# Kernel tuning notes

Measured on AMD Instinct MI355X. Metric: run time of the kernel, lower is better.

Reference implementation:

```python
import math
import jax, jax.numpy as jnp
import numpy as np

ROUTER_TEMP = 1.5
CAP_FACTOR = 1.25  # training capacity factor
NUM_EXPERTS = 16


def setup_inputs() -> dict:
    key = jax.random.key(0)
    k1, k2 = jax.random.split(key)
    N, C, H, W = 8192, 64, 8, 8
    E = NUM_EXPERTS
    X = jax.random.normal(k1, (N, C, H, W), dtype=jnp.float32)
    Wg = jax.random.normal(k2, (C, E), dtype=jnp.float32) * (1.0 / np.sqrt(C))
    bg = jnp.zeros((E,), dtype=jnp.float32)
    return {"X": X, "Wg": Wg, "bg": bg}


def reference(X, Wg, bg):
    N, C, H, W = X.shape
    E = Wg.shape[1]

    # router_gate: global average pool over (H, W) then Linear(C -> E)
    pooled = X.mean(axis=(2, 3))                       # [N, C]
    raw_logits = pooled @ Wg + bg                      # [N, E]
    logits = jnp.clip(raw_logits.astype(jnp.float32) / ROUTER_TEMP, -10.0, 10.0)
    logits_std = jnp.std(logits)

    # z-loss: mean of squared logsumexp over experts
    z_loss = jnp.mean(jnp.square(jax.nn.logsumexp(logits, axis=-1)))

    probs = jax.nn.softmax(logits, axis=1)             # [N, E]
    expert_idx = jnp.argmax(probs, axis=1)             # [N]
    expert_prob = jnp.take_along_axis(probs, expert_idx[:, None], axis=1)[:, 0]  # [N]
    expert_mask = jax.nn.one_hot(expert_idx, E, dtype=probs.dtype)               # [N, E]

    Ccap = int(max(1, math.ceil(CAP_FACTOR * N / E)))  # static capacity per expert

    # sort tokens by gate probability (descending), capacity-mask via cumsum
    order = jnp.argsort(-expert_prob)                  # [N]
    mask_sorted = expert_mask[order].astype(jnp.int32) # [N, E]
    pos_sorted = jnp.cumsum(mask_sorted, axis=0) - 1   # position within expert
    within_cap = (pos_sorted >= 0) & (pos_sorted < Ccap)
    mask_sorted = (mask_sorted.astype(bool) & within_cap).astype(jnp.int32)

    unsort = jnp.argsort(order)                        # inverse permutation
    mask = mask_sorted[unsort].astype(probs.dtype)     # [N, E]

    # aux load-balancing loss
    aux_loss = jnp.sum(mask.mean(axis=0) * probs.mean(axis=0)) * E

    # combine weights: gate prob normalized over (top-1) surviving experts
    raw = mask * expert_prob[:, None]                  # [N, E]
    denom = jax.lax.stop_gradient(jnp.clip(raw.sum(axis=1, keepdims=True), 1e-6, None))
    w = raw / denom

    pos_idx = jnp.clip(pos_sorted, 0, Ccap - 1)[unsort]          # [N, E]
    one_hot_pos = jax.nn.one_hot(pos_idx, Ccap, dtype=mask.dtype)  # [N, E, Ccap]
    combine = (w[:, :, None] * one_hot_pos).astype(X.dtype)        # [N, E, Ccap]
    dispatch = mask[:, :, None].astype(bool) & one_hot_pos.astype(bool)

    return dispatch, combine, z_loss, aux_loss, logits_std, logits
```

## Files before the change

### kernel.cpp

```cpp
#include <hip/hip_runtime.h>
#include <math.h>

#define NTOK 8192
#define NE   16
#define CAP  640
#define EC   (NE * CAP)

constexpr size_t DISP_SZ  = (size_t)NTOK * EC;
constexpr size_t SCAL_OFF = 2 * DISP_SZ;
constexpr size_t LOG_OFF  = SCAL_OFF + 3;

#define WS_KEY 0
#define WS_PD  65536
#define WS_PI  376832

__global__ __launch_bounds__(256) void k_router(
    const float4* __restrict__ X4, const float* __restrict__ Wg,
    const float* __restrict__ bg, float* __restrict__ out,
    unsigned long long* __restrict__ key,
    double* __restrict__ pD, int* __restrict__ pI)
{
    __shared__ double sPex[4][NE];
    __shared__ float  sLog[4][NE];
    __shared__ double sLse[4];
    __shared__ int    sExp[4];

    const int tid = threadIdx.x;
    const int w   = tid >> 6;
    const int l   = tid & 63;
    const int n   = blockIdx.x * 4 + w;
    const int e   = l & 15;
    const int g   = l >> 4;

    float wreg[16];
#pragma unroll
    for (int i = 0; i < 16; i++)
        wreg[i] = Wg[(16 * g + i) * 16 + e];

    const float4* xb = X4 + (size_t)n * 1024;
    double dot = 0.0;
#pragma unroll
    for (int i = 0; i < 16; i++) {
        float4 v = xb[g * 256 + i * 16 + e];
        double s4 = ((double)v.x + (double)v.y) + ((double)v.z + (double)v.w);
        s4 += __shfl_xor(s4, 1, 64);
        s4 += __shfl_xor(s4, 2, 64);
        s4 += __shfl_xor(s4, 4, 64);
        s4 += __shfl_xor(s4, 8, 64);
        float pooled = (float)(s4 * (1.0 / 64.0));
        dot += (double)pooled * (double)wreg[i];
    }
    dot += __shfl_xor(dot, 16, 64);
    dot += __shfl_xor(dot, 32, 64);

    float raw = (float)dot + bg[e];
    float lg  = raw / 1.5f;
    lg = fminf(fmaxf(lg, -10.0f), 10.0f);

    float mv = lg; int mi = e;
#pragma unroll
    for (int off = 1; off <= 8; off <<= 1) {
        float ov = __shfl_xor(mv, off, 64);
        int   oi = __shfl_xor(mi, off, 64);
        if (ov > mv || (ov == mv && oi < mi)) { mv = ov; mi = oi; }
    }

    float d  = lg - mv;
    float ex = (float)exp((double)d);
    double sd = (double)ex;
#pragma unroll
    for (int off = 1; off <= 8; off <<= 1)
        sd += __shfl_xor(sd, off, 64);
    float sumf = (float)sd;
    float ptop = 1.0f / sumf;
    double lse = (double)mv + log(sd);

    unsigned int pb = __float_as_uint(ptop);
    unsigned long long kk = ((unsigned long long)mi << 43)
                          | ((unsigned long long)pb << 13)
                          | (unsigned long long)(8191 - n);

    if (l == 0) { key[n] = kk; sLse[w] = lse; sExp[w] = mi; }
    if (l < 16) {
        out[LOG_OFF + (size_t)n * 16 + e] = lg;
        sPex[w][e] = (double)ex / sd;
        sLog[w][e] = lg;
    }
    __syncthreads();

    if (tid < 16) {
        pD[blockIdx.x * 19 + 3 + tid] =
            sPex[0][tid] + sPex[1][tid] + sPex[2][tid] + sPex[3][tid];
        pI[blockIdx.x * 16 + tid] = (sExp[0] == tid) + (sExp[1] == tid)
                                  + (sExp[2] == tid) + (sExp[3] == tid);
    } else if (tid == 16) {
        double z = 0.0;
        for (int i = 0; i < 4; i++) z += sLse[i] * sLse[i];
        pD[blockIdx.x * 19 + 0] = z;
    } else if (tid == 17) {
        double s = 0.0;
        for (int i = 0; i < 4; i++)
            for (int j = 0; j < 16; j++) s += (double)sLog[i][j];
        pD[blockIdx.x * 19 + 1] = s;
    } else if (tid == 18) {
        double s = 0.0;
        for (int i = 0; i < 4; i++)
            for (int j = 0; j < 16; j++) {
                double v = (double)sLog[i][j]; s += v * v;
            }
        pD[blockIdx.x * 19 + 2] = s;
    }
}

__global__ __launch_bounds__(256) void k_rank(
    const unsigned long long* __restrict__ key, float* __restrict__ out)
{
    const int tid = threadIdx.x;
    const int tok = blockIdx.x * 8 + (tid >> 5);
    const int sub = tid & 31;
    const unsigned long long me = key[tok];
    const unsigned long long my_e = me >> 43;

    int cnt = 0;
    for (int m = sub; m < NTOK; m += 32) {
        unsigned long long km = key[m];
        cnt += ((km >> 43) == my_e && km > me) ? 1 : 0;
    }
#pragma unroll
    for (int off = 16; off >= 1; off >>= 1)
        cnt += __shfl_down(cnt, off, 32);

    if (sub == 0 && cnt < CAP) {
        size_t idx = (size_t)tok * EC + (size_t)my_e * CAP + (size_t)cnt;
        out[idx] = 1.0f;
        out[DISP_SZ + idx] = 1.0f;
    }
}

__global__ __launch_bounds__(256) void k_finalize(
    const double* __restrict__ pD, const int* __restrict__ pI,
    float* __restrict__ out)
{
    __shared__ double sD[256][20];
    __shared__ int    sI[256][NE];
    const int t = threadIdx.x;

    double a[19];
#pragma unroll
    for (int f = 0; f < 19; f++) a[f] = 0.0;
    int ci[NE];
#pragma unroll
    for (int f = 0; f < NE; f++) ci[f] = 0;

    for (int b = t; b < 2048; b += 256) {
        const double* rowD = pD + b * 19;
#pragma unroll
        for (int f = 0; f < 19; f++) a[f] += rowD[f];
        const int* rowI = pI + b * NE;
#pragma unroll
        for (int f = 0; f < NE; f++) ci[f] += rowI[f];
    }
#pragma unroll
    for (int f = 0; f < 19; f++) sD[t][f] = a[f];
#pragma unroll
    for (int f = 0; f < NE; f++) sI[t][f] = ci[f];
    __syncthreads();

    if (t == 0) {
        double tot[19];
        for (int f = 0; f < 19; f++) tot[f] = 0.0;
        int totI[NE];
        for (int f = 0; f < NE; f++) totI[f] = 0;
        for (int i = 0; i < 256; i++) {
            for (int f = 0; f < 19; f++) tot[f] += sD[i][f];
            for (int f = 0; f < NE; f++) totI[f] += sI[i][f];
        }
        double z = tot[0] / (double)NTOK;
        double aux = 0.0;
        for (int e = 0; e < NE; e++) {
            int kept = totI[e] < CAP ? totI[e] : CAP;
            aux += ((double)kept / (double)NTOK) * (tot[3 + e] / (double)NTOK);
        }
        aux *= (double)NE;
        double cntall = (double)NTOK * NE;
        double mean = tot[1] / cntall;
        double var  = tot[2] / cntall - mean * mean;
        if (var < 0.0) var = 0.0;
        out[SCAL_OFF + 0] = (float)z;
        out[SCAL_OFF + 1] = (float)aux;
        out[SCAL_OFF + 2] = (float)sqrt(var);
    }
}

extern "C" void kernel_launch(void* const* d_in, const int* in_sizes, int n_in,
                              void* d_out, int out_size, void* d_ws, size_t ws_size,
                              hipStream_t stream)
{
    const float* X  = (const float*)d_in[0];
    const float* Wg = (const float*)d_in[1];
    const float* bg = (const float*)d_in[2];
    float* out = (float*)d_out;

    char* ws = (char*)d_ws;
    unsigned long long* key = (unsigned long long*)(ws + WS_KEY);
    double* pD = (double*)(ws + WS_PD);
    int*    pI = (int*)   (ws + WS_PI);

    hipMemsetAsync(d_out, 0, (size_t)out_size * sizeof(float), stream);

    k_router<<<NTOK / 4, 256, 0, stream>>>((const float4*)X, Wg, bg, out,
                                           key, pD, pI);
    k_rank<<<NTOK / 8, 256, 0, stream>>>(key, out);
    k_finalize<<<1, 256, 0, stream>>>(pD, pI, out);
}
```

Baseline: 843.5 us.

## Fuse output zeroing into router kernel and merge rank with finalize

Drops the separate hipMemsetAsync. Extra blocks appended to the router launch now zero the dispatch and combine regions, so that zeroing runs alongside the X pooling and routing work. The rank kernel first stages all 8192 keys in shared memory instead of rereading them from global memory for every token, and the finalize reduction becomes an extra block of that same launch, which cuts one kernel launch. The 64KB shared buffer per block limits how many rank blocks can sit on a CU at once, and the custom zeroing may not match the store throughput of the driver memset.

Measured after the change: 823.3 us. 1.02x faster.

```diff
diff --git a/kernel.cpp b/kernel.cpp
--- a/kernel.cpp
+++ b/kernel.cpp
@@ -14,18 +14,31 @@
 #define WS_PD  65536
 #define WS_PI  376832
 
-__global__ __launch_bounds__(256) void k_router(
+#define NZBLK 10240
+#define NRBLK 2048
+
+__global__ __launch_bounds__(256) void k_main(
     const float4* __restrict__ X4, const float* __restrict__ Wg,
     const float* __restrict__ bg, float* __restrict__ out,
     unsigned long long* __restrict__ key,
     double* __restrict__ pD, int* __restrict__ pI)
 {
+    const int tid = threadIdx.x;
+
+    if (blockIdx.x >= NRBLK) {
+        float4* o4 = (float4*)out + (size_t)(blockIdx.x - NRBLK) * 4096;
+        const float4 z = make_float4(0.f, 0.f, 0.f, 0.f);
+#pragma unroll
+        for (int k = 0; k < 16; k++)
+            o4[tid + 256 * k] = z;
+        return;
+    }
+
     __shared__ double sPex[4][NE];
     __shared__ float  sLog[4][NE];
     __shared__ double sLse[4];
     __shared__ int    sExp[4];
 
-    const int tid = threadIdx.x;
     const int w   = tid >> 6;
     const int l   = tid & 63;
     const int n   = blockIdx.x * 4 + w;
@@ -112,39 +125,43 @@
     }
 }
 
-__global__ __launch_bounds__(256) void k_rank(
-    const unsigned long long* __restrict__ key, float* __restrict__ out)
-{
-    const int tid = threadIdx.x;
-    const int tok = blockIdx.x * 8 + (tid >> 5);
-    const int sub = tid & 31;
-    const unsigned long long me = key[tok];
-    const unsigned long long my_e = me >> 43;
-
-    int cnt = 0;
-    for (int m = sub; m < NTOK; m += 32) {
-        unsigned long long km = key[m];
-        cnt += ((km >> 43) == my_e && km > me) ? 1 : 0;
-    }
-#pragma unroll
-    for (int off = 16; off >= 1; off >>= 1)
-        cnt += __shfl_down(cnt, off, 32);
-
-    if (sub == 0 && cnt < CAP) {
-        size_t idx = (size_t)tok * EC + (size_t)my_e * CAP + (size_t)cnt;
-        out[idx] = 1.0f;
-        out[DISP_SZ + idx] = 1.0f;
-    }
-}
-
-__global__ __launch_bounds__(256) void k_finalize(
+__global__ __launch_bounds__(256) void k_scatter(
+    const unsigned long long* __restrict__ key,
     const double* __restrict__ pD, const int* __restrict__ pI,
     float* __restrict__ out)
 {
-    __shared__ double sD[256][20];
-    __shared__ int    sI[256][NE];
-    const int t = threadIdx.x;
-
+    __shared__ unsigned long long skey[NTOK];
+    const int tid = threadIdx.x;
+
+    if (blockIdx.x < 1024) {
+        for (int k = 0; k < 32; k++)
+            skey[tid + 256 * k] = key[tid + 256 * k];
+        __syncthreads();
+
+        const int tok = blockIdx.x * 8 + (tid >> 5);
+        const int sub = tid & 31;
+        const unsigned long long me = skey[tok];
+        const unsigned long long my_e = me >> 43;
+
+        int cnt = 0;
+        for (int m = sub; m < NTOK; m += 32) {
+            unsigned long long km = skey[m];
+            cnt += ((km >> 43) == my_e && km > me) ? 1 : 0;
+        }
+#pragma unroll
+        for (int off = 16; off >= 1; off >>= 1)
+            cnt += __shfl_down(cnt, off, 32);
+
+        if (sub == 0 && cnt < CAP) {
+            size_t idx = (size_t)tok * EC + (size_t)my_e * CAP + (size_t)cnt;
+            out[idx] = 1.0f;
+            out[DISP_SZ + idx] = 1.0f;
+        }
+        return;
+    }
+
+    double* sD = (double*)skey;
+    int*    sI = (int*)(skey + 5120);
     double a[19];
 #pragma unroll
     for (int f = 0; f < 19; f++) a[f] = 0.0;
@@ -152,7 +169,7 @@
 #pragma unroll
     for (int f = 0; f < NE; f++) ci[f] = 0;
 
-    for (int b = t; b < 2048; b += 256) {
+    for (int b = tid; b < 2048; b += 256) {
         const double* rowD = pD + b * 19;
 #pragma unroll
         for (int f = 0; f < 19; f++) a[f] += rowD[f];
@@ -161,19 +178,19 @@
         for (int f = 0; f < NE; f++) ci[f] += rowI[f];
     }
 #pragma unroll
-    for (int f = 0; f < 19; f++) sD[t][f] = a[f];
-#pragma unroll
-    for (int f = 0; f < NE; f++) sI[t][f] = ci[f];
+    for (int f = 0; f < 19; f++) sD[tid * 20 + f] = a[f];
+#pragma unroll
+    for (int f = 0; f < NE; f++) sI[tid * 16 + f] = ci[f];
     __syncthreads();
 
-    if (t == 0) {
+    if (tid == 0) {
         double tot[19];
         for (int f = 0; f < 19; f++) tot[f] = 0.0;
         int totI[NE];
         for (int f = 0; f < NE; f++) totI[f] = 0;
         for (int i = 0; i < 256; i++) {
-            for (int f = 0; f < 19; f++) tot[f] += sD[i][f];
-            for (int f = 0; f < NE; f++) totI[f] += sI[i][f];
+            for (int f = 0; f < 19; f++) tot[f] += sD[i * 20 + f];
+            for (int f = 0; f < NE; f++) totI[f] += sI[i * 16 + f];
         }
         double z = tot[0] / (double)NTOK;
         double aux = 0.0;
@@ -206,10 +223,7 @@
     double* pD = (double*)(ws + WS_PD);
     int*    pI = (int*)   (ws + WS_PI);
 
-    hipMemsetAsync(d_out, 0, (size_t)out_size * sizeof(float), stream);
-
-    k_router<<<NTOK / 4, 256, 0, stream>>>((const float4*)X, Wg, bg, out,
-                                           key, pD, pI);
-    k_rank<<<NTOK / 8, 256, 0, stream>>>(key, out);
-    k_finalize<<<1, 256, 0, stream>>>(pD, pI, out);
+    k_main<<<NRBLK + NZBLK, 256, 0, stream>>>((const float4*)X, Wg, bg, out,
+                                              key, pD, pI);
+    k_scatter<<<1025, 256, 0, stream>>>(key, pD, pI, out);
 }
```
